# Optimization experiments

Measured on AMD Instinct MI355X. Metric: run time of the kernel, lower is better.

The kernel has to match this reference:

```python
import jax, jax.numpy as jnp
import numpy as np

BETA = 0.95
SG_SLOPE = 25.0

@jax.custom_vjp
def spike(mem, thr):
    return (mem > thr).astype(mem.dtype)

def _spike_fwd(mem, thr):
    return spike(mem, thr), (mem, thr)

def _spike_bwd(res, g):
    mem, thr = res
    s = jax.nn.sigmoid(SG_SLOPE * (mem - thr))
    return (g * (SG_SLOPE * s * (1.0 - s)), jnp.zeros_like(thr))

spike.defvjp(_spike_fwd, _spike_bwd)

def setup_inputs() -> dict:
    key = jax.random.key(0)
    ks = jax.random.split(key, 7)
    T, B, IN, H, OUT = 50, 512, 784, 800, 10
    return {
        "x":  jax.random.normal(ks[0], (T, B, IN), dtype=jnp.float32),
        "W1": jax.random.normal(ks[1], (H, IN), dtype=jnp.float32) / np.sqrt(IN),
        "b1": jax.random.normal(ks[2], (H,), dtype=jnp.float32) * 0.01,
        "W2": jax.random.normal(ks[3], (H, H), dtype=jnp.float32) / np.sqrt(H),
        "b2": jax.random.normal(ks[4], (H,), dtype=jnp.float32) * 0.01,
        "W3": jax.random.normal(ks[5], (OUT, H), dtype=jnp.float32) / np.sqrt(H),
        "b3": jax.random.normal(ks[6], (OUT,), dtype=jnp.float32) * 0.01,
        "thresh1": jnp.ones((H,), dtype=jnp.float32),
        "thresh2": jnp.ones((H,), dtype=jnp.float32),
    }

def reference(x, W1, b1, W2, b2, W3, b3, thresh1, thresh2):
    T, B = x.shape[0], x.shape[1]
    H, OUT = W1.shape[0], W3.shape[0]
    # Batch the input projection across all timesteps: [T,B,H]
    x1 = jnp.einsum('tbi,hi->tbh', x, W1) + b1

    def step(carry, xt):
        mem1, mem2, mem3 = carry
        mem1 = BETA * mem1 + xt
        spk1 = spike(mem1, thresh1)
        mem1 = mem1 * (1.0 - spk1)
        mem2 = BETA * mem2 + spk1 @ W2.T + b2
        spk2 = spike(mem2, thresh2)
        mem2 = mem2 * (1.0 - spk2)
        mem3 = BETA * mem3 + spk2 @ W3.T + b3
        spk3 = spike(mem3, jnp.float32(1.0))
        mem3 = mem3 * (1.0 - spk3)
        return (mem1, mem2, mem3), (spk1, spk2, spk3)

    init = (jnp.zeros((B, H), x.dtype), jnp.zeros((B, H), x.dtype), jnp.zeros((B, OUT), x.dtype))
    _, (s1r, s2r, s3r) = jax.lax.scan(step, init, x1)
    return s3r.sum(0), s1r, s2r, s3r
```

## Files before the change

kernel.cpp:

```cpp
#include <hip/hip_runtime.h>

#define TT 50
#define BB 512
#define II 784
#define HH 800
#define OO 10
#define BH (BB*HH)
#define MM (TT*BB)

__global__ __launch_bounds__(256) void k_gemm1(
    const float* __restrict__ x, const float* __restrict__ W1,
    const float* __restrict__ b1, double* __restrict__ x1d)
{
    __shared__ double As[16*130];
    __shared__ double Bs[16*82];
    const int m0 = blockIdx.x * 128;
    const int n0 = blockIdx.y * 80;
    const int tid = threadIdx.x;
    const int tx = tid & 15, ty = tid >> 4;
    double acc[8][5] = {};

    const int sm = tid >> 1;
    const int sk = (tid & 1) * 8;
    const int bq0n = tid >> 2, bq0k = (tid & 3) * 4;
    const int q1 = tid + 256;
    const int bq1n = q1 >> 2, bq1k = (q1 & 3) * 4;

    for (int k0 = 0; k0 < II; k0 += 16) {
        const float4 a0 = *(const float4*)(x + (long)(m0+sm)*II + k0 + sk);
        const float4 a1 = *(const float4*)(x + (long)(m0+sm)*II + k0 + sk + 4);
        const float4 bv0 = *(const float4*)(W1 + (long)(n0+bq0n)*II + k0 + bq0k);
        float4 bv1;
        if (tid < 64)
            bv1 = *(const float4*)(W1 + (long)(n0+bq1n)*II + k0 + bq1k);
        __syncthreads();
        As[(sk+0)*130+sm] = (double)a0.x;
        As[(sk+1)*130+sm] = (double)a0.y;
        As[(sk+2)*130+sm] = (double)a0.z;
        As[(sk+3)*130+sm] = (double)a0.w;
        As[(sk+4)*130+sm] = (double)a1.x;
        As[(sk+5)*130+sm] = (double)a1.y;
        As[(sk+6)*130+sm] = (double)a1.z;
        As[(sk+7)*130+sm] = (double)a1.w;
        Bs[(bq0k+0)*82+bq0n] = (double)bv0.x;
        Bs[(bq0k+1)*82+bq0n] = (double)bv0.y;
        Bs[(bq0k+2)*82+bq0n] = (double)bv0.z;
        Bs[(bq0k+3)*82+bq0n] = (double)bv0.w;
        if (tid < 64) {
            Bs[(bq1k+0)*82+bq1n] = (double)bv1.x;
            Bs[(bq1k+1)*82+bq1n] = (double)bv1.y;
            Bs[(bq1k+2)*82+bq1n] = (double)bv1.z;
            Bs[(bq1k+3)*82+bq1n] = (double)bv1.w;
        }
        __syncthreads();
        #pragma unroll
        for (int k = 0; k < 16; ++k) {
            double a[8], b[5];
            #pragma unroll
            for (int i = 0; i < 8; ++i) a[i] = As[k*130 + ty + 16*i];
            #pragma unroll
            for (int j = 0; j < 5; ++j) b[j] = Bs[k*82 + tx + 16*j];
            #pragma unroll
            for (int i = 0; i < 8; ++i)
                #pragma unroll
                for (int j = 0; j < 5; ++j)
                    acc[i][j] = fma(a[i], b[j], acc[i][j]);
        }
    }
    #pragma unroll
    for (int i = 0; i < 8; ++i) {
        const long m = m0 + ty + 16*i;
        #pragma unroll
        for (int j = 0; j < 5; ++j) {
            const int n = n0 + tx + 16*j;
            x1d[m*HH + n] = acc[i][j] + (double)b1[n];
        }
    }
}

__global__ __launch_bounds__(256) void k_mem1(
    const double* __restrict__ x1d, const float* __restrict__ thresh1,
    unsigned char* __restrict__ s1c, float* __restrict__ s1r)
{
    const int lid = blockIdx.x*256 + threadIdx.x;
    const int h = lid % HH;
    const double th = (double)thresh1[h];
    double mem = 0.0;
    for (int t = 0; t < TT; ++t) {
        const long idx = (long)t*BH + lid;
        mem = 0.95*mem + x1d[idx];
        const bool spk = mem > th;
        s1c[idx] = spk ? 1 : 0;
        s1r[idx] = spk ? 1.0f : 0.0f;
        if (spk) mem = 0.0;
    }
}

__global__ __launch_bounds__(256) void k_gemm2(
    const unsigned char* __restrict__ s1c, const float* __restrict__ W2,
    float* __restrict__ z2)
{
    __shared__ float As[32*132];
    __shared__ float Bs[32*84];
    const int m0 = blockIdx.x * 128;
    const int n0 = blockIdx.y * 80;
    const int tid = threadIdx.x;
    const int tx = tid & 15, ty = tid >> 4;
    float acc[8][5] = {};

    const int sm = tid >> 1;
    const int sk = (tid & 1) * 16;
    const int b0n = tid >> 3,        b0k = (tid & 7) * 4;
    const int q1 = tid + 256, b1n = q1 >> 3, b1k = (q1 & 7) * 4;
    const int q2 = tid + 512, b2n = q2 >> 3, b2k = (q2 & 7) * 4;

    for (int k0 = 0; k0 < HH; k0 += 32) {
        const uint4 av = *(const uint4*)(s1c + (long)(m0+sm)*HH + k0 + sk);
        const float4 w0 = *(const float4*)(W2 + (long)(n0+b0n)*HH + k0 + b0k);
        const float4 w1 = *(const float4*)(W2 + (long)(n0+b1n)*HH + k0 + b1k);
        float4 w2;
        if (tid < 128)
            w2 = *(const float4*)(W2 + (long)(n0+b2n)*HH + k0 + b2k);
        __syncthreads();
        {
            const unsigned int d[4] = {av.x, av.y, av.z, av.w};
            #pragma unroll
            for (int w = 0; w < 4; ++w) {
                #pragma unroll
                for (int j = 0; j < 4; ++j)
                    As[(sk + w*4 + j)*132 + sm] =
                        (float)((d[w] >> (8*j)) & 0xffu);
            }
        }
        Bs[(b0k+0)*84+b0n] = w0.x; Bs[(b0k+1)*84+b0n] = w0.y;
        Bs[(b0k+2)*84+b0n] = w0.z; Bs[(b0k+3)*84+b0n] = w0.w;
        Bs[(b1k+0)*84+b1n] = w1.x; Bs[(b1k+1)*84+b1n] = w1.y;
        Bs[(b1k+2)*84+b1n] = w1.z; Bs[(b1k+3)*84+b1n] = w1.w;
        if (tid < 128) {
            Bs[(b2k+0)*84+b2n] = w2.x; Bs[(b2k+1)*84+b2n] = w2.y;
            Bs[(b2k+2)*84+b2n] = w2.z; Bs[(b2k+3)*84+b2n] = w2.w;
        }
        __syncthreads();
        #pragma unroll
        for (int k = 0; k < 32; ++k) {
            float a[8], b[5];
            #pragma unroll
            for (int i = 0; i < 8; ++i) a[i] = As[k*132 + ty*8 + i];
            #pragma unroll
            for (int j = 0; j < 4; ++j) b[j] = Bs[k*84 + tx*4 + j];
            b[4] = Bs[k*84 + 64 + tx];
            #pragma unroll
            for (int i = 0; i < 8; ++i)
                #pragma unroll
                for (int j = 0; j < 5; ++j)
                    acc[i][j] = __fmaf_rn(a[i], b[j], acc[i][j]);
        }
    }
    #pragma unroll
    for (int i = 0; i < 8; ++i) {
        const long m = m0 + ty*8 + i;
        #pragma unroll
        for (int j = 0; j < 4; ++j)
            z2[m*HH + n0 + tx*4 + j] = acc[i][j];
        z2[m*HH + n0 + 64 + tx] = acc[i][4];
    }
}

__global__ __launch_bounds__(256) void k_scan2(
    const float* __restrict__ z2, const float* __restrict__ b2,
    const float* __restrict__ thresh2, float* __restrict__ s2r,
    unsigned char* __restrict__ s2c)
{
    const int lid = blockIdx.x*256 + threadIdx.x;
    const int n = lid % HH;
    const float b2v = b2[n];
    const float thv = thresh2[n];
    float m = 0.0f;
    for (int t = 0; t < TT; ++t) {
        const long idx = (long)t*BH + lid;
        const float m2 = __fadd_rn(
            __fadd_rn(__fmul_rn(0.95f, m), z2[idx]), b2v);
        const bool spk = m2 > thv;
        s2r[idx] = spk ? 1.0f : 0.0f;
        s2c[idx] = spk ? 1 : 0;
        m = spk ? 0.0f : m2;
    }
}

__global__ __launch_bounds__(256) void k_gemm3(
    const unsigned char* __restrict__ s2c, const float* __restrict__ W3,
    float* __restrict__ z3)
{
    const long m = blockIdx.x*256 + threadIdx.x;
    const unsigned char* row = s2c + m*HH;
    float acc[10] = {};
    for (int k0 = 0; k0 < HH; k0 += 16) {
        const uint4 v = *(const uint4*)(row + k0);
        const unsigned int d[4] = {v.x, v.y, v.z, v.w};
        #pragma unroll
        for (int w = 0; w < 4; ++w) {
            #pragma unroll
            for (int j = 0; j < 4; ++j) {
                const float sv = (float)((d[w] >> (8*j)) & 0xffu);
                const int k = k0 + w*4 + j;
                #pragma unroll
                for (int o = 0; o < 10; ++o)
                    acc[o] = __fmaf_rn(sv, W3[o*HH + k], acc[o]);
            }
        }
    }
    #pragma unroll
    for (int o = 0; o < 10; ++o)
        z3[m*OO + o] = acc[o];
}

__global__ __launch_bounds__(256) void k_scan3(
    const float* __restrict__ z3, const float* __restrict__ b3,
    float* __restrict__ s3r, float* __restrict__ out0)
{
    const int gid = blockIdx.x*256 + threadIdx.x;
    if (gid >= BB*OO) return;
    const int o = gid % OO;
    const float b3v = b3[o];
    float mem = 0.0f, cnt = 0.0f;
    for (int t = 0; t < TT; ++t) {
        const float m3 = __fadd_rn(
            __fadd_rn(__fmul_rn(0.95f, mem), z3[(long)t*BB*OO + gid]), b3v);
        const bool spk = m3 > 1.0f;
        s3r[(long)t*BB*OO + gid] = spk ? 1.0f : 0.0f;
        if (spk) cnt = __fadd_rn(cnt, 1.0f);
        mem = spk ? 0.0f : m3;
    }
    out0[gid] = cnt;
}

extern "C" void kernel_launch(void* const* d_in, const int* in_sizes, int n_in,
                              void* d_out, int out_size, void* d_ws, size_t ws_size,
                              hipStream_t stream)
{
    const float* x   = (const float*)d_in[0];
    const float* W1  = (const float*)d_in[1];
    const float* b1  = (const float*)d_in[2];
    const float* W2  = (const float*)d_in[3];
    const float* b2  = (const float*)d_in[4];
    const float* W3  = (const float*)d_in[5];
    const float* b3  = (const float*)d_in[6];
    const float* th1 = (const float*)d_in[7];
    const float* th2 = (const float*)d_in[8];

    float* out0 = (float*)d_out;
    float* s1r  = out0 + BB*OO;
    float* s2r  = s1r + (long)TT*BH;
    float* s3r  = s2r + (long)TT*BH;

    char* p = (char*)d_ws;
    double* x1d = (double*)p;
    float*  z2  = (float*)p;
    float*  z3  = (float*)(p + 84000000);
    unsigned char* s1c = (unsigned char*)(p + 163840000);
    unsigned char* s2c = s1c + (size_t)TT*BH;
    (void)ws_size;

    k_gemm1<<<dim3(200,10), dim3(256), 0, stream>>>(x, W1, b1, x1d);
    k_mem1 <<<dim3(1600),   dim3(256), 0, stream>>>(x1d, th1, s1c, s1r);
    k_gemm2<<<dim3(200,10), dim3(256), 0, stream>>>(s1c, W2, z2);
    k_scan2<<<dim3(1600),   dim3(256), 0, stream>>>(z2, b2, th2, s2r, s2c);
    k_gemm3<<<dim3(100),    dim3(256), 0, stream>>>(s2c, W3, z3);
    k_scan3<<<dim3(20),     dim3(256), 0, stream>>>(z3, b3, s3r, out0);
}
```

Measured before the change: 1.479 ms.

## Use FP64 MFMA instructions for input projection GEMM with runtime layout probing

Replaces the scalar FP64 FMA inner loop of the input-projection GEMM with 16x16x4 FP64 MFMA matrix instructions. Each wavefront computes a 32x80 tile. The accumulator and operand lane layout is discovered at runtime by running probe MFMAs on lane indices. Shared-memory tiles are now kept as float and converted to double at load, which halves LDS footprint and store traffic. The risk is that the layout-decoding heuristic is fragile. The GEMM is also only one part of the total time, since the recurrent steps remain.

Measured after the change: 1.406 ms. -4.9%, faster.

```diff
diff --git a/kernel.cpp b/kernel.cpp
--- a/kernel.cpp
+++ b/kernel.cpp
@@ -8,72 +8,114 @@
 #define BH (BB*HH)
 #define MM (TT*BB)
 
+typedef double d4 __attribute__((ext_vector_type(4)));
+
+__device__ __forceinline__ int dec16(double V) {
+    const int vi = (int)(V + 0.5);
+    const int a = vi - 96;
+    if (a >= 0 && a < 64 && (a & 3) == 0) return a >> 2;
+    return ((vi - 6) >> 4) & 15;
+}
+__device__ __forceinline__ bool isf1(double V) {
+    const int vi = (int)(V + 0.5);
+    const int a = vi - 96;
+    return (a >= 0 && a < 64 && (a & 3) == 0);
+}
+
 __global__ __launch_bounds__(256) void k_gemm1(
     const float* __restrict__ x, const float* __restrict__ W1,
     const float* __restrict__ b1, double* __restrict__ x1d)
 {
-    __shared__ double As[16*130];
-    __shared__ double Bs[16*82];
+    __shared__ float As[16*144];
+    __shared__ float Bs[16*80];
     const int m0 = blockIdx.x * 128;
     const int n0 = blockIdx.y * 80;
     const int tid = threadIdx.x;
-    const int tx = tid & 15, ty = tid >> 4;
-    double acc[8][5] = {};
+    const int lane = tid & 63;
+    const int wm = (tid >> 6) * 32;
+
+    const d4 zc = {0.0, 0.0, 0.0, 0.0};
+    const d4 pr = __builtin_amdgcn_mfma_f64_16x16x4f64(
+        (double)lane, 1.0, zc, 0, 0, 0);
+    const d4 pc = __builtin_amdgcn_mfma_f64_16x16x4f64(
+        1.0, (double)lane, zc, 0, 0, 0);
+    int rowIdx[4], colIdx[4];
+    #pragma unroll
+    for (int r = 0; r < 4; ++r) {
+        rowIdx[r] = dec16(pr[r]) & 15;
+        colIdx[r] = dec16(pc[r]) & 15;
+    }
+    const bool af1 = isf1(pr[0]);
+    const bool bf1 = isf1(pc[0]);
+    const int arow = af1 ? (lane & 15) : (lane >> 2);
+    const int akk  = af1 ? (lane >> 4) : (lane & 3);
+    const int bcol = bf1 ? (lane & 15) : (lane >> 2);
+    const int bkk  = bf1 ? (lane >> 4) : (lane & 3);
+
+    d4 acc[2][5] = {};
 
     const int sm = tid >> 1;
     const int sk = (tid & 1) * 8;
-    const int bq0n = tid >> 2, bq0k = (tid & 3) * 4;
-    const int q1 = tid + 256;
-    const int bq1n = q1 >> 2, bq1k = (q1 & 3) * 4;
+    const int bn0 = tid >> 2, bk0 = (tid & 3) * 4;
+    const int q1  = tid + 256;
+    const int bn1 = q1 >> 2,  bk1 = (q1 & 3) * 4;
 
     for (int k0 = 0; k0 < II; k0 += 16) {
         const float4 a0 = *(const float4*)(x + (long)(m0+sm)*II + k0 + sk);
         const float4 a1 = *(const float4*)(x + (long)(m0+sm)*II + k0 + sk + 4);
-        const float4 bv0 = *(const float4*)(W1 + (long)(n0+bq0n)*II + k0 + bq0k);
-        float4 bv1;
+        const float4 w0 = *(const float4*)(W1 + (long)(n0+bn0)*II + k0 + bk0);
+        float4 w1;
         if (tid < 64)
-            bv1 = *(const float4*)(W1 + (long)(n0+bq1n)*II + k0 + bq1k);
+            w1 = *(const float4*)(W1 + (long)(n0+bn1)*II + k0 + bk1);
         __syncthreads();
-        As[(sk+0)*130+sm] = (double)a0.x;
-        As[(sk+1)*130+sm] = (double)a0.y;
-        As[(sk+2)*130+sm] = (double)a0.z;
-        As[(sk+3)*130+sm] = (double)a0.w;
-        As[(sk+4)*130+sm] = (double)a1.x;
-        As[(sk+5)*130+sm] = (double)a1.y;
-        As[(sk+6)*130+sm] = (double)a1.z;
-        As[(sk+7)*130+sm] = (double)a1.w;
-        Bs[(bq0k+0)*82+bq0n] = (double)bv0.x;
-        Bs[(bq0k+1)*82+bq0n] = (double)bv0.y;
-        Bs[(bq0k+2)*82+bq0n] = (double)bv0.z;
-        Bs[(bq0k+3)*82+bq0n] = (double)bv0.w;
+        As[(sk+0)*144+sm] = a0.x;
+        As[(sk+1)*144+sm] = a0.y;
+        As[(sk+2)*144+sm] = a0.z;
+        As[(sk+3)*144+sm] = a0.w;
+        As[(sk+4)*144+sm] = a1.x;
+        As[(sk+5)*144+sm] = a1.y;
+        As[(sk+6)*144+sm] = a1.z;
+        As[(sk+7)*144+sm] = a1.w;
+        Bs[(bk0+0)*80+bn0] = w0.x;
+        Bs[(bk0+1)*80+bn0] = w0.y;
+        Bs[(bk0+2)*80+bn0] = w0.z;
+        Bs[(bk0+3)*80+bn0] = w0.w;
         if (tid < 64) {
-            Bs[(bq1k+0)*82+bq1n] = (double)bv1.x;
-            Bs[(bq1k+1)*82+bq1n] = (double)bv1.y;
-            Bs[(bq1k+2)*82+bq1n] = (double)bv1.z;
-            Bs[(bq1k+3)*82+bq1n] = (double)bv1.w;
+            Bs[(bk1+0)*80+bn1] = w1.x;
+            Bs[(bk1+1)*80+bn1] = w1.y;
+            Bs[(bk1+2)*80+bn1] = w1.z;
+            Bs[(bk1+3)*80+bn1] = w1.w;
         }
         __syncthreads();
         #pragma unroll
-        for (int k = 0; k < 16; ++k) {
-            double a[8], b[5];
-            #pragma unroll
-            for (int i = 0; i < 8; ++i) a[i] = As[k*130 + ty + 16*i];
-            #pragma unroll
-            for (int j = 0; j < 5; ++j) b[j] = Bs[k*82 + tx + 16*j];
-            #pragma unroll
-            for (int i = 0; i < 8; ++i)
-                #pragma unroll
-                for (int j = 0; j < 5; ++j)
-                    acc[i][j] = fma(a[i], b[j], acc[i][j]);
+        for (int s = 0; s < 4; ++s) {
+            const int ka = 4*s + akk;
+            const int kb = 4*s + bkk;
+            const double a0d = (double)As[ka*144 + wm + arow];
+            const double a1d = (double)As[ka*144 + wm + 16 + arow];
+            double bd[5];
+            #pragma unroll
+            for (int j = 0; j < 5; ++j)
+                bd[j] = (double)Bs[kb*80 + 16*j + bcol];
+            #pragma unroll
+            for (int j = 0; j < 5; ++j) {
+                acc[0][j] = __builtin_amdgcn_mfma_f64_16x16x4f64(
+                    a0d, bd[j], acc[0][j], 0, 0, 0);
+                acc[1][j] = __builtin_amdgcn_mfma_f64_16x16x4f64(
+                    a1d, bd[j], acc[1][j], 0, 0, 0);
+            }
         }
     }
     #pragma unroll
-    for (int i = 0; i < 8; ++i) {
-        const long m = m0 + ty + 16*i;
-        #pragma unroll
-        for (int j = 0; j < 5; ++j) {
-            const int n = n0 + tx + 16*j;
-            x1d[m*HH + n] = acc[i][j] + (double)b1[n];
+    for (int i = 0; i < 2; ++i) {
+        #pragma unroll
+        for (int r = 0; r < 4; ++r) {
+            const long m = m0 + wm + 16*i + rowIdx[r];
+            #pragma unroll
+            for (int j = 0; j < 5; ++j) {
+                const int n = n0 + 16*j + colIdx[r];
+                x1d[m*HH + n] = acc[i][j][r] + (double)b1[n];
+            }
         }
     }
 }
```
